# Kernel tuning notes

Measured on AMD Instinct MI355X. Metric: run time of the kernel, lower is better.

## Reference

```python
import jax, jax.numpy as jnp
import numpy as np

H, NH, NKV, HD = 4096, 32, 8, 128
GROUPS = NH // NKV            # 4
QKV_OUT = (NH + 2 * NKV) * HD # 6144
LORA_R = 256
SCALING = 1.0                 # lora_alpha / lora_r = 256/256
BLOCK_SIZE = 64


def rotate_half(x):
    d = x.shape[-1] // 2
    return jnp.concatenate([-x[..., d:], x[..., :d]], axis=-1)


def apply_rope(x, cos, sin):
    # x: [T, heads, HD]; cos/sin: [T, HD]
    return x * cos[:, None, :] + rotate_half(x) * sin[:, None, :]


def plora(x2d, w, A, B, MA, MB, im_idx, mem_idx):
    # x2d: [T, in]; w: [out, in]; A:[r,in] B:[out,r]; MA:[256,in] MB:[out,256]
    res = x2d @ w.T
    lora_im = (x2d[im_idx] @ A.T) @ B.T
    res = res.at[im_idx].add(SCALING * lora_im)
    lora_mem = (x2d[mem_idx] @ MA.T) @ MB.T
    res = res.at[mem_idx].add(SCALING * lora_mem)
    return res


def setup_inputs() -> dict:
    key = jax.random.key(0)
    ks = jax.random.split(key, 20)
    T = 2048
    inp = {
        'hidden_states': jax.random.normal(ks[0], (1, T, H), jnp.float32),
        'cos': jax.random.uniform(ks[1], (T, HD), jnp.float32, -1.0, 1.0),
        'sin': jax.random.uniform(ks[2], (T, HD), jnp.float32, -1.0, 1.0),
        'beacon_cos': jax.random.uniform(ks[3], (128, HD), jnp.float32, -1.0, 1.0),
        'beacon_sin': jax.random.uniform(ks[4], (128, HD), jnp.float32, -1.0, 1.0),
        'mem_idx': jax.random.randint(ks[5], (128,), 0, T, jnp.int32),
        'im_idx': jax.random.randint(ks[6], (512,), 0, T, jnp.int32),
        'k_cache': jnp.zeros((4, BLOCK_SIZE, NKV, HD), jnp.float32),
        'v_cache': jnp.zeros((4, BLOCK_SIZE, NKV, HD), jnp.float32),
        'block_offsets': jnp.arange(2, dtype=jnp.int32).reshape(1, 2),
        'wqkv_w': jax.random.normal(ks[7], (QKV_OUT, H), jnp.float32) * 0.02,
        'wqkv_A': jax.random.normal(ks[8], (LORA_R, H), jnp.float32) * 0.02,
        'wqkv_B': jax.random.normal(ks[9], (QKV_OUT, LORA_R), jnp.float32) * 0.02,
        'wqkv_MA': jax.random.normal(ks[10], (256, H), jnp.float32) * 0.02,
        'wqkv_MB': jax.random.normal(ks[11], (QKV_OUT, 256), jnp.float32) * 0.02,
        'wo_w': jax.random.normal(ks[12], (H, NH * HD), jnp.float32) * 0.02,
        'wo_A': jax.random.normal(ks[13], (LORA_R, NH * HD), jnp.float32) * 0.02,
        'wo_B': jax.random.normal(ks[14], (H, LORA_R), jnp.float32) * 0.02,
        'wo_MA': jax.random.normal(ks[15], (256, NH * HD), jnp.float32) * 0.02,
        'wo_MB': jax.random.normal(ks[16], (H, 256), jnp.float32) * 0.02,
    }
    return inp


def reference(hidden_states, cos, sin, beacon_cos, beacon_sin, mem_idx, im_idx,
              k_cache, v_cache, block_offsets,
              wqkv_w, wqkv_A, wqkv_B, wqkv_MA, wqkv_MB,
              wo_w, wo_A, wo_B, wo_MA, wo_MB):
    Bsz, N, C = hidden_states.shape
    x = hidden_states.reshape(-1, C)  # [T, H]
    T = x.shape[0]

    # ---- wqkv PLoRA ----
    qkv = plora(x, wqkv_w, wqkv_A, wqkv_B, wqkv_MA, wqkv_MB, im_idx, mem_idx)
    qkv = qkv.reshape(T, NKV, 2 + GROUPS, HD)
    q = qkv[:, :, :GROUPS, :].reshape(T, NH, HD)   # [T, 32, 128]
    k = qkv[:, :, -2, :]                           # [T, 8, 128]
    v = qkv[:, :, -1, :]                           # [T, 8, 128]

    # ---- fill_kv_cache: beacon tokens with beacon RoPE -> paged cache ----
    fill_k = apply_rope(k[mem_idx], beacon_cos, beacon_sin)  # [M, 8, 128]
    fill_v = v[mem_idx]
    M = fill_k.shape[0]
    pos = jnp.arange(M)
    blk = block_offsets[0, pos // BLOCK_SIZE]
    off = pos % BLOCK_SIZE
    k_cache_new = k_cache.at[blk, off].set(fill_k)
    v_cache_new = v_cache.at[blk, off].set(fill_v)

    # ---- RoPE on q/k ----
    q = apply_rope(q, cos, sin)
    k = apply_rope(k, cos, sin)

    # ---- causal GQA flash attention (single varlen sequence of length T) ----
    qg = q.reshape(T, NKV, GROUPS, HD)
    scale = 1.0 / np.sqrt(HD)
    scores = jnp.einsum('qhgd,shd->hgqs', qg, k) * scale  # [8,4,T,T]
    causal = jnp.tril(jnp.ones((T, T), dtype=bool))
    scores = jnp.where(causal[None, None], scores, jnp.finfo(scores.dtype).min)
    probs = jax.nn.softmax(scores, axis=-1)
    attn = jnp.einsum('hgqs,shd->qhgd', probs, v).reshape(T, NH * HD)

    # ---- wo PLoRA ----
    out = plora(attn, wo_w, wo_A, wo_B, wo_MA, wo_MB, im_idx, mem_idx)
    out = out.reshape(Bsz, N, H)
    return out, k_cache_new, v_cache_new
```

## Files before the change

kernel.cpp:

```cpp
#include <hip/hip_runtime.h>
#include <hip/hip_bf16.h>
#include <stdint.h>

typedef __bf16 bf16;
typedef __bf16 bf16x8 __attribute__((ext_vector_type(8)));
typedef float f32x4 __attribute__((ext_vector_type(4)));

#define T_SEQ 2048
#define NH 32
#define NKV 8
#define HD 128
#define HDIM 4096
#define QKV_OUT 6144

__device__ __forceinline__ void g2l16(const void* g, void* l) {
  __builtin_amdgcn_global_load_lds(
      (const __attribute__((address_space(1))) void*)g,
      (__attribute__((address_space(3))) void*)l, 16, 0, 0);
}

__global__ __launch_bounds__(256) void cvt_kernel(const float* __restrict__ in,
                                                  bf16* __restrict__ out, int n) {
  int stride = gridDim.x * blockDim.x * 8;
  for (int i = (blockIdx.x * blockDim.x + threadIdx.x) * 8; i < n; i += stride) {
    float4 a = *(const float4*)(in + i);
    float4 b = *(const float4*)(in + i + 4);
    bf16x8 o;
    o[0] = (bf16)a.x; o[1] = (bf16)a.y; o[2] = (bf16)a.z; o[3] = (bf16)a.w;
    o[4] = (bf16)b.x; o[5] = (bf16)b.y; o[6] = (bf16)b.z; o[7] = (bf16)b.w;
    *(bf16x8*)(out + i) = o;
  }
}

__global__ __launch_bounds__(256) void zero_f32(float* __restrict__ p, int n) {
  int i = blockIdx.x * 256 + threadIdx.x;
  if (i < n) p[i] = 0.f;
}

__global__ __launch_bounds__(256)
void gemm128(const bf16* __restrict__ A, const bf16* __restrict__ B,
             float* __restrict__ C, int M, int N, int K) {
  __shared__ bf16 As[128 * 32];
  __shared__ bf16 Bs[128 * 32];
  const int tid = threadIdx.x;
  const int wid = tid >> 6, lane = tid & 63;
  const int bm = blockIdx.x * 128, bn = blockIdx.y * 128;
  const int wr = (wid >> 1) * 64, wc = (wid & 1) * 64;
  const int lr = lane & 15, lk = (lane >> 4) * 8;
  const int srow = wid * 32 + (lane >> 2);
  const int scol = (lane & 3) * 8;
  const bf16* Ag = A + (size_t)(bm + srow) * K + scol;
  const bf16* Bg = B + (size_t)(bn + srow) * K + scol;
  bf16* Al = As + wid * 1024;
  bf16* Bl = Bs + wid * 1024;
  f32x4 acc[4][4] = {};
  for (int k0 = 0; k0 < K; k0 += 32) {
    g2l16(Ag + k0, Al);
    g2l16(Ag + k0 + (size_t)16 * K, Al + 512);
    g2l16(Bg + k0, Bl);
    g2l16(Bg + k0 + (size_t)16 * K, Bl + 512);
    __syncthreads();
    bf16x8 af[4], bfv[4];
#pragma unroll
    for (int m = 0; m < 4; ++m)
      af[m] = *(const bf16x8*)(As + (wr + m * 16 + lr) * 32 + lk);
#pragma unroll
    for (int n = 0; n < 4; ++n)
      bfv[n] = *(const bf16x8*)(Bs + (wc + n * 16 + lr) * 32 + lk);
#pragma unroll
    for (int m = 0; m < 4; ++m)
#pragma unroll
      for (int n = 0; n < 4; ++n)
        acc[m][n] = __builtin_amdgcn_mfma_f32_16x16x32_bf16(af[m], bfv[n], acc[m][n], 0, 0, 0);
    __syncthreads();
  }
  const int orow = (lane >> 4) * 4;
#pragma unroll
  for (int m = 0; m < 4; ++m)
#pragma unroll
    for (int n = 0; n < 4; ++n)
#pragma unroll
      for (int j = 0; j < 4; ++j)
        C[(size_t)(bm + wr + m * 16 + orow + j) * N + (bn + wc + n * 16 + lr)] = acc[m][n][j];
}

template <int GATHER_A, int MODE>
__global__ __launch_bounds__(256)
void gemm64(const bf16* __restrict__ A, const bf16* __restrict__ B,
            const int* __restrict__ aidx, const int* __restrict__ cidx,
            bf16* __restrict__ outb, float* __restrict__ outf,
            int M, int N, int K, int ldc, float alpha) {
  __shared__ bf16 As[64 * 32];
  __shared__ bf16 Bs[64 * 32];
  const int tid = threadIdx.x;
  const int wid = tid >> 6, lane = tid & 63;
  const int bm = blockIdx.x * 64, bn = blockIdx.y * 64;
  const int wr = (wid >> 1) * 32, wc = (wid & 1) * 32;
  const int lr = lane & 15, lk = (lane >> 4) * 8;
  int arow = bm + wid * 16 + (lane >> 2);
  if (GATHER_A) arow = aidx[arow];
  const int scol = (lane & 3) * 8;
  const bf16* Ag = A + (size_t)arow * K + scol;
  const bf16* Bg = B + (size_t)(bn + wid * 16 + (lane >> 2)) * K + scol;
  bf16* Al = As + wid * 512;
  bf16* Bl = Bs + wid * 512;
  int kbeg = 0, kend = K;
  if (MODE == 2) { int kc = K / gridDim.z; kbeg = blockIdx.z * kc; kend = kbeg + kc; }
  f32x4 acc[2][2] = {};
  for (int k0 = kbeg; k0 < kend; k0 += 32) {
    g2l16(Ag + k0, Al);
    g2l16(Bg + k0, Bl);
    __syncthreads();
    bf16x8 af[2], bfv[2];
#pragma unroll
    for (int m = 0; m < 2; ++m)
      af[m] = *(const bf16x8*)(As + (wr + m * 16 + lr) * 32 + lk);
#pragma unroll
    for (int n = 0; n < 2; ++n)
      bfv[n] = *(const bf16x8*)(Bs + (wc + n * 16 + lr) * 32 + lk);
#pragma unroll
    for (int m = 0; m < 2; ++m)
#pragma unroll
      for (int n = 0; n < 2; ++n)
        acc[m][n] = __builtin_amdgcn_mfma_f32_16x16x32_bf16(af[m], bfv[n], acc[m][n], 0, 0, 0);
    __syncthreads();
  }
  const int orow = (lane >> 4) * 4;
#pragma unroll
  for (int m = 0; m < 2; ++m)
#pragma unroll
    for (int n = 0; n < 2; ++n)
#pragma unroll
      for (int j = 0; j < 4; ++j) {
        int r = bm + wr + m * 16 + orow + j;
        int c = bn + wc + n * 16 + lr;
        float v = acc[m][n][j];
        if (MODE == 0)      outb[(size_t)r * ldc + c] = (bf16)(v * alpha);
        else if (MODE == 1) atomicAdd(outf + (size_t)cidx[r] * ldc + c, v * alpha);
        else                atomicAdd(outf + (size_t)r * ldc + c, v);
      }
}

__global__ __launch_bounds__(256)
void rope_q(const float* __restrict__ qkv, const float* __restrict__ cosp,
            const float* __restrict__ sinp, bf16* __restrict__ qb) {
  int idx = blockIdx.x * 4 + (threadIdx.x >> 6);
  int d = threadIdx.x & 63;
  int t = idx >> 5, h = idx & 31;
  const float* src = qkv + (size_t)t * QKV_OUT + (h >> 2) * 768 + (h & 3) * 128;
  float x0 = src[d], x1 = src[d + 64];
  float c0 = cosp[t * HD + d], c1 = cosp[t * HD + d + 64];
  float s0 = sinp[t * HD + d], s1 = sinp[t * HD + d + 64];
  const float SC = 0.08838834764831845f * 1.4426950408889634f;
  bf16* dst = qb + ((size_t)t * NH + h) * HD;
  dst[d]      = (bf16)((x0 * c0 - x1 * s0) * SC);
  dst[d + 64] = (bf16)((x1 * c1 + x0 * s1) * SC);
}

__global__ __launch_bounds__(256)
void rope_k(const float* __restrict__ qkv, const float* __restrict__ cosp,
            const float* __restrict__ sinp, bf16* __restrict__ kb) {
  int idx = blockIdx.x * 4 + (threadIdx.x >> 6);
  int d = threadIdx.x & 63;
  int t = idx >> 3, kvh = idx & 7;
  const float* src = qkv + (size_t)t * QKV_OUT + kvh * 768 + 512;
  float x0 = src[d], x1 = src[d + 64];
  float c0 = cosp[t * HD + d], c1 = cosp[t * HD + d + 64];
  float s0 = sinp[t * HD + d], s1 = sinp[t * HD + d + 64];
  bf16* dst = kb + ((size_t)t * NKV + kvh) * HD;
  dst[d]      = (bf16)(x0 * c0 - x1 * s0);
  dst[d + 64] = (bf16)(x1 * c1 + x0 * s1);
}

__global__ __launch_bounds__(256)
void v_trans(const float* __restrict__ qkv, bf16* __restrict__ vtb) {
  __shared__ bf16 tile[128][72];
  const int kvh = blockIdx.y;
  const int t0 = blockIdx.x * 64;
  const int tid = threadIdx.x;
  for (int i = tid; i < 64 * 32; i += 256) {
    int t = i >> 5;
    int dq = (i & 31) * 4;
    const float* p = qkv + (size_t)(t0 + t) * QKV_OUT + kvh * 768 + 640 + dq;
    float4 v = *(const float4*)p;
    tile[dq + 0][t] = (bf16)v.x;
    tile[dq + 1][t] = (bf16)v.y;
    tile[dq + 2][t] = (bf16)v.z;
    tile[dq + 3][t] = (bf16)v.w;
  }
  __syncthreads();
  for (int i = tid; i < 128 * 8; i += 256) {
    int d = i >> 3;
    int tt = (i & 7) * 8;
    bf16x8 v;
#pragma unroll
    for (int j = 0; j < 8; ++j) v[j] = tile[d][tt + j];
    *(bf16x8*)(vtb + ((size_t)kvh * HD + d) * T_SEQ + t0 + tt) = v;
  }
}

__global__ __launch_bounds__(256)
void cache_copy(const float* __restrict__ kc, const float* __restrict__ vc,
                float* __restrict__ kout, float* __restrict__ vout) {
  int i = blockIdx.x * 256 + threadIdx.x;
  kout[i] = kc[i];
  vout[i] = vc[i];
}

__global__ __launch_bounds__(256)
void cache_fill(const float* __restrict__ qkv, const int* __restrict__ mem_idx,
                const int* __restrict__ blk_off, const float* __restrict__ bcos,
                const float* __restrict__ bsin,
                float* __restrict__ kout, float* __restrict__ vout) {
  const int m = blockIdx.x;
  const int row = mem_idx[m];
  const int blk = blk_off[m >> 6];
  const int off = m & 63;
  const int tid = threadIdx.x;
  for (int i = tid; i < NKV * 64; i += 256) {
    int kvh = i >> 6, d = i & 63;
    const float* ks = qkv + (size_t)row * QKV_OUT + kvh * 768 + 512;
    const float* vs = ks + 128;
    float x0 = ks[d], x1 = ks[d + 64];
    float c0 = bcos[m * HD + d], c1 = bcos[m * HD + d + 64];
    float s0 = bsin[m * HD + d], s1 = bsin[m * HD + d + 64];
    size_t base = (((size_t)blk * 64 + off) * NKV + kvh) * HD;
    kout[base + d]      = x0 * c0 - x1 * s0;
    kout[base + d + 64] = x1 * c1 + x0 * s1;
    vout[base + d]      = vs[d];
    vout[base + d + 64] = vs[d + 64];
  }
}

__global__ __launch_bounds__(256)
void flash(const bf16* __restrict__ qb, const bf16* __restrict__ kb,
           const bf16* __restrict__ vtb, bf16* __restrict__ attnb) {
  __shared__ bf16 Ks[32 * 128];
  __shared__ bf16 Vs[128 * 32];
  __shared__ bf16 Ps[4][16 * 32];
  const int q0 = blockIdx.x * 64;
  const int h = blockIdx.y;
  const int kvh = h >> 2;
  const int tid = threadIdx.x;
  const int wid = tid >> 6, lane = tid & 63;
  const int lr = lane & 15, lg = lane >> 4;
  const int lk = lg * 8;
  bf16x8 qf[4];
  {
    const bf16* qsrc = qb + (((size_t)(q0 + wid * 16 + lr)) * NH + h) * HD + lk;
#pragma unroll
    for (int kk = 0; kk < 4; ++kk) qf[kk] = *(const bf16x8*)(qsrc + kk * 32);
  }
  f32x4 o[8] = {};
  float mrow[4] = {-1e30f, -1e30f, -1e30f, -1e30f};
  float lrow[4] = {0.f, 0.f, 0.f, 0.f};
  const int kv_end = q0 + 64;
  const int krr = wid * 8 + lg;
  const int kcb = lr * 16;
  const int vdr = wid * 32 + (lane >> 2);
  const int vcb = (lane & 3) * 16;
  for (int jt = 0; jt < kv_end; jt += 32) {
    {
      int d0 = (kcb ^ ((krr & 7) << 4)) >> 1;
      g2l16(kb + ((size_t)(jt + krr) * NKV + kvh) * HD + d0, Ks + wid * 1024);
      int rr1 = krr + 4;
      int d1 = (kcb ^ ((rr1 & 7) << 4)) >> 1;
      g2l16(kb + ((size_t)(jt + rr1) * NKV + kvh) * HD + d1, Ks + wid * 1024 + 512);
      int t0 = (vcb ^ (((vdr >> 1) & 3) << 4)) >> 1;
      g2l16(vtb + ((size_t)kvh * HD + vdr) * T_SEQ + jt + t0, Vs + wid * 1024);
      int vdr1 = vdr + 16;
      int t1 = (vcb ^ (((vdr1 >> 1) & 3) << 4)) >> 1;
      g2l16(vtb + ((size_t)kvh * HD + vdr1) * T_SEQ + jt + t1, Vs + wid * 1024 + 512);
    }
    __syncthreads();
    f32x4 S[2] = {};
    const char* KsB = (const char*)Ks;
#pragma unroll
    for (int ch = 0; ch < 2; ++ch) {
      int row = ch * 16 + lr;
      int rbase = row * 256;
      int swz = (row & 7) << 4;
#pragma unroll
      for (int kk = 0; kk < 4; ++kk) {
        bf16x8 kf = *(const bf16x8*)(KsB + rbase + ((kk * 64 + lg * 16) ^ swz));
        S[ch] = __builtin_amdgcn_mfma_f32_16x16x32_bf16(qf[kk], kf, S[ch], 0, 0, 0);
      }
    }
    const int baserow = q0 + wid * 16 + lg * 4;
    float corr[4];
#pragma unroll
    for (int j = 0; j < 4; ++j) {
      int row = baserow + j;
      float s0 = (jt + lr <= row)      ? S[0][j] : -1e30f;
      float s1 = (jt + 16 + lr <= row) ? S[1][j] : -1e30f;
      float tmx = fmaxf(s0, s1);
#pragma unroll
      for (int off = 1; off < 16; off <<= 1)
        tmx = fmaxf(tmx, __shfl_xor(tmx, off, 64));
      float mn = fmaxf(mrow[j], tmx);
      corr[j] = exp2f(mrow[j] - mn);
      mrow[j] = mn;
      float p0 = (s0 <= -1e29f) ? 0.f : exp2f(s0 - mn);
      float p1 = (s1 <= -1e29f) ? 0.f : exp2f(s1 - mn);
      S[0][j] = p0; S[1][j] = p1;
      float ps = p0 + p1;
#pragma unroll
      for (int off = 1; off < 16; off <<= 1)
        ps += __shfl_xor(ps, off, 64);
      lrow[j] = lrow[j] * corr[j] + ps;
    }
#pragma unroll
    for (int db = 0; db < 8; ++db) {
      o[db][0] *= corr[0]; o[db][1] *= corr[1];
      o[db][2] *= corr[2]; o[db][3] *= corr[3];
    }
    bf16* pw = Ps[wid];
#pragma unroll
    for (int j = 0; j < 4; ++j) {
      pw[(lg * 4 + j) * 32 + lr]      = (bf16)S[0][j];
      pw[(lg * 4 + j) * 32 + 16 + lr] = (bf16)S[1][j];
    }
    asm volatile("s_waitcnt lgkmcnt(0)" ::: "memory");
    bf16x8 pa = *(const bf16x8*)(pw + lr * 32 + lk);
    const char* VsB = (const char*)Vs;
    int vswz = ((lr >> 1) & 3) << 4;
#pragma unroll
    for (int db = 0; db < 8; ++db) {
      bf16x8 vf = *(const bf16x8*)(VsB + (db * 16 + lr) * 64 + ((lg * 16) ^ vswz));
      o[db] = __builtin_amdgcn_mfma_f32_16x16x32_bf16(pa, vf, o[db], 0, 0, 0);
    }
    __syncthreads();
  }
#pragma unroll
  for (int j = 0; j < 4; ++j) {
    float inv = 1.f / lrow[j];
    bf16* od = attnb + (((size_t)(q0 + wid * 16 + lg * 4 + j)) * NH + h) * HD;
#pragma unroll
    for (int db = 0; db < 8; ++db)
      od[db * 16 + lr] = (bf16)(o[db][j] * inv);
  }
}

extern "C" void kernel_launch(void* const* d_in, const int* in_sizes, int n_in,
                              void* d_out, int out_size, void* d_ws, size_t ws_size,
                              hipStream_t stream) {
  (void)in_sizes; (void)n_in; (void)out_size; (void)ws_size;
  const float* hidden  = (const float*)d_in[0];
  const float* cosp    = (const float*)d_in[1];
  const float* sinp    = (const float*)d_in[2];
  const float* bcos    = (const float*)d_in[3];
  const float* bsin    = (const float*)d_in[4];
  const int*   mem_idx = (const int*)d_in[5];
  const int*   im_idx  = (const int*)d_in[6];
  const float* kc_in   = (const float*)d_in[7];
  const float* vc_in   = (const float*)d_in[8];
  const int*   blk_off = (const int*)d_in[9];
  const float* wqkv_w  = (const float*)d_in[10];
  const float* wqkv_A  = (const float*)d_in[11];
  const float* wqkv_B  = (const float*)d_in[12];
  const float* wqkv_MA = (const float*)d_in[13];
  const float* wqkv_MB = (const float*)d_in[14];
  const float* wo_w    = (const float*)d_in[15];
  const float* wo_A    = (const float*)d_in[16];
  const float* wo_B    = (const float*)d_in[17];
  const float* wo_MA   = (const float*)d_in[18];
  const float* wo_MB   = (const float*)d_in[19];

  char* ws = (char*)d_ws;
  size_t off = 0;
  auto alloc = [&](size_t b) { char* p = ws + off; off += (b + 255) & ~(size_t)255; return p; };
  bf16* xb    = (bf16*)alloc(2048ull * 4096 * 2);
  bf16* wqkvb = (bf16*)alloc(6144ull * 4096 * 2);
  bf16* wob   = (bf16*)alloc(4096ull * 4096 * 2);
  bf16* qAb   = (bf16*)alloc(256ull * 4096 * 2);
  bf16* qBb   = (bf16*)alloc(6144ull * 256 * 2);
  bf16* qMAb  = (bf16*)alloc(256ull * 4096 * 2);
  bf16* qMBb  = (bf16*)alloc(6144ull * 256 * 2);
  bf16* oAb   = (bf16*)alloc(256ull * 4096 * 2);
  bf16* oBb   = (bf16*)alloc(4096ull * 256 * 2);
  bf16* oMAb  = (bf16*)alloc(256ull * 4096 * 2);
  bf16* oMBb  = (bf16*)alloc(4096ull * 256 * 2);
  float* qkv  = (float*)alloc(2048ull * 6144 * 4);
  bf16* qb    = (bf16*)alloc(2048ull * 32 * 128 * 2);
  bf16* kbuf  = (bf16*)alloc(2048ull * 8 * 128 * 2);
  bf16* vtb   = (bf16*)alloc(8ull * 128 * 2048 * 2);
  bf16* attnb = (bf16*)alloc(2048ull * 4096 * 2);
  float* tf   = (float*)alloc(1280ull * 256 * 4);
  bf16* tb    = (bf16*)alloc(1280ull * 256 * 2);
  float* t_im_f  = tf;               float* t_mem_f  = tf + 512 * 256;
  float* t2_im_f = tf + 640 * 256;   float* t2_mem_f = tf + 1152 * 256;
  bf16* t_im_b   = tb;               bf16* t_mem_b   = tb + 512 * 256;
  bf16* t2_im_b  = tb + 640 * 256;   bf16* t2_mem_b  = tb + 1152 * 256;
  (void)t_mem_f; (void)t2_mem_f;

  float* outp   = (float*)d_out;
  float* kc_out = outp + 2048ull * 4096;
  float* vc_out = kc_out + 4ull * 64 * 8 * 128;

  auto cvt = [&](const float* src, bf16* dst, size_t n) {
    size_t g = (n / 8 + 255) / 256;
    if (g > 2048) g = 2048;
    cvt_kernel<<<(unsigned)g, 256, 0, stream>>>(src, dst, (int)n);
  };
  cvt(hidden, xb, 2048ull * 4096);
  cvt(wqkv_w, wqkvb, 6144ull * 4096);
  cvt(wo_w, wob, 4096ull * 4096);
  cvt(wqkv_A, qAb, 256ull * 4096);
  cvt(wqkv_B, qBb, 6144ull * 256);
  cvt(wqkv_MA, qMAb, 256ull * 4096);
  cvt(wqkv_MB, qMBb, 6144ull * 256);
  cvt(wo_A, oAb, 256ull * 4096);
  cvt(wo_B, oBb, 4096ull * 256);
  cvt(wo_MA, oMAb, 256ull * 4096);
  cvt(wo_MB, oMBb, 4096ull * 256);
  zero_f32<<<1280, 256, 0, stream>>>(tf, 1280 * 256);

  gemm128<<<dim3(16, 48), 256, 0, stream>>>(xb, wqkvb, qkv, 2048, 6144, 4096);
  gemm64<1, 2><<<dim3(8, 4, 8), 256, 0, stream>>>(xb, qAb, im_idx, nullptr, nullptr, t_im_f, 512, 256, 4096, 256, 1.f);
  gemm64<1, 2><<<dim3(2, 4, 8), 256, 0, stream>>>(xb, qMAb, mem_idx, nullptr, nullptr, t_mem_f, 128, 256, 4096, 256, 1.f);
  cvt(tf, tb, 640 * 256);
  gemm64<0, 1><<<dim3(8, 96), 256, 0, stream>>>(t_im_b, qBb, nullptr, im_idx, nullptr, qkv, 512, 6144, 256, 6144, 1.f);
  gemm64<0, 1><<<dim3(2, 96), 256, 0, stream>>>(t_mem_b, qMBb, nullptr, mem_idx, nullptr, qkv, 128, 6144, 256, 6144, 1.f);

  rope_q<<<16384, 256, 0, stream>>>(qkv, cosp, sinp, qb);
  rope_k<<<4096, 256, 0, stream>>>(qkv, cosp, sinp, kbuf);
  v_trans<<<dim3(32, 8), 256, 0, stream>>>(qkv, vtb);
  cache_copy<<<1024, 256, 0, stream>>>(kc_in, vc_in, kc_out, vc_out);
  cache_fill<<<128, 256, 0, stream>>>(qkv, mem_idx, blk_off, bcos, bsin, kc_out, vc_out);

  flash<<<dim3(32, 32), 256, 0, stream>>>(qb, kbuf, vtb, attnb);

  gemm128<<<dim3(16, 32), 256, 0, stream>>>(attnb, wob, outp, 2048, 4096, 4096);
  gemm64<1, 2><<<dim3(8, 4, 8), 256, 0, stream>>>(attnb, oAb, im_idx, nullptr, nullptr, t2_im_f, 512, 256, 4096, 256, 1.f);
  gemm64<1, 2><<<dim3(2, 4, 8), 256, 0, stream>>>(attnb, oMAb, mem_idx, nullptr, nullptr, t2_mem_f, 128, 256, 4096, 256, 1.f);
  cvt(t2_im_f, t2_im_b, 640 * 256);
  gemm64<0, 1><<<dim3(8, 64), 256, 0, stream>>>(t2_im_b, oBb, nullptr, im_idx, nullptr, outp, 512, 4096, 256, 4096, 1.f);
  gemm64<0, 1><<<dim3(2, 64), 256, 0, stream>>>(t2_mem_b, oMBb, nullptr, mem_idx, nullptr, outp, 128, 4096, 256, 4096, 1.f);
}
```

Before: 913.2 us.

## Restructure flash attention with 128-row Q tiles, 64-key blocks and register P

The flash attention kernel now gives each block 128 query rows (32 per wave, as two 16-row sub-tiles) and loads 64 keys per iteration, so each K/V tile in shared memory is reused by twice as many rows. It computes S transposed (K times Q), so every lane owns one query row and softmax reductions need only two cross-lane shuffles. The probability tile is repacked into the MFMA operand layout with register shuffles rather than a round trip through shared memory. Blocks run the heaviest causal tiles first, waves skip fully masked key blocks, and masking is applied only on diagonal tiles. The trade-offs are higher register pressure and half as many blocks in the grid.

```diff
diff --git a/kernel.cpp b/kernel.cpp
--- a/kernel.cpp
+++ b/kernel.cpp
@@ -4,6 +4,7 @@
 
 typedef __bf16 bf16;
 typedef __bf16 bf16x8 __attribute__((ext_vector_type(8)));
+typedef __bf16 bf16x4 __attribute__((ext_vector_type(4)));
 typedef float f32x4 __attribute__((ext_vector_type(4)));
 
 #define T_SEQ 2048
@@ -232,112 +233,166 @@
   }
 }
 
+__device__ __forceinline__ uint32_t pk2(float x, float y) {
+  bf16 a = (bf16)x, b = (bf16)y;
+  uint16_t ua = __builtin_bit_cast(uint16_t, a), ub = __builtin_bit_cast(uint16_t, b);
+  return (uint32_t)ua | ((uint32_t)ub << 16);
+}
+
+__device__ __forceinline__ bf16x8 dance(const f32x4& pc0, const f32x4& pc1, int lg) {
+  uint32_t a0 = pk2(pc0[0], pc0[1]), a1 = pk2(pc0[2], pc0[3]);
+  uint32_t b0 = pk2(pc1[0], pc1[1]), b1 = pk2(pc1[2], pc1[3]);
+  bool lo = lg < 2;
+  uint32_t k0 = lo ? a0 : b0, k1 = lo ? a1 : b1;
+  uint32_t s0 = lo ? b0 : a0, s1 = lo ? b1 : a1;
+  uint32_t r0 = (uint32_t)__shfl_xor((int)s0, 32, 64);
+  uint32_t r1 = (uint32_t)__shfl_xor((int)s1, 32, 64);
+  uint32_t tk0 = (uint32_t)__shfl_xor((int)k0, 16, 64);
+  uint32_t tk1 = (uint32_t)__shfl_xor((int)k1, 16, 64);
+  uint32_t tr0 = (uint32_t)__shfl_xor((int)r0, 16, 64);
+  uint32_t tr1 = (uint32_t)__shfl_xor((int)r1, 16, 64);
+  bool ev = !(lg & 1);
+  union { uint32_t u[4]; bf16x8 v; } out;
+  out.u[0] = ev ? (lo ? k0 : r0) : (lo ? tr0 : tk0);
+  out.u[1] = ev ? (lo ? k1 : r1) : (lo ? tr1 : tk1);
+  out.u[2] = ev ? (lo ? tk0 : tr0) : (lo ? r0 : k0);
+  out.u[3] = ev ? (lo ? tk1 : tr1) : (lo ? r1 : k1);
+  return out.v;
+}
+
+__device__ __forceinline__ float online_sm(f32x4 (&S)[4], float& m_r, float& l_r) {
+  float pmax = S[0][0];
+#pragma unroll
+  for (int ch = 0; ch < 4; ++ch)
+#pragma unroll
+    for (int j = 0; j < 4; ++j) pmax = fmaxf(pmax, S[ch][j]);
+  pmax = fmaxf(pmax, __shfl_xor(pmax, 16, 64));
+  pmax = fmaxf(pmax, __shfl_xor(pmax, 32, 64));
+  float mn = fmaxf(m_r, pmax);
+  float corr = exp2f(m_r - mn);
+  m_r = mn;
+  float ps = 0.f;
+#pragma unroll
+  for (int ch = 0; ch < 4; ++ch)
+#pragma unroll
+    for (int j = 0; j < 4; ++j) {
+      float p = exp2f(S[ch][j] - mn);
+      S[ch][j] = p;
+      ps += p;
+    }
+  ps += __shfl_xor(ps, 16, 64);
+  ps += __shfl_xor(ps, 32, 64);
+  l_r = l_r * corr + ps;
+  return corr;
+}
+
 __global__ __launch_bounds__(256)
 void flash(const bf16* __restrict__ qb, const bf16* __restrict__ kb,
            const bf16* __restrict__ vtb, bf16* __restrict__ attnb) {
-  __shared__ bf16 Ks[32 * 128];
-  __shared__ bf16 Vs[128 * 32];
-  __shared__ bf16 Ps[4][16 * 32];
-  const int q0 = blockIdx.x * 64;
+  __shared__ bf16 Ks[64 * 128];
+  __shared__ bf16 Vs[128 * 64];
+  const int qt = gridDim.x - 1 - blockIdx.x;
+  const int q0 = qt * 128;
   const int h = blockIdx.y;
   const int kvh = h >> 2;
   const int tid = threadIdx.x;
   const int wid = tid >> 6, lane = tid & 63;
   const int lr = lane & 15, lg = lane >> 4;
-  const int lk = lg * 8;
-  bf16x8 qf[4];
+  const int qrowA = q0 + wid * 32 + lr;
+  const int qrowB = qrowA + 16;
+
+  bf16x8 qfA[4], qfB[4];
   {
-    const bf16* qsrc = qb + (((size_t)(q0 + wid * 16 + lr)) * NH + h) * HD + lk;
-#pragma unroll
-    for (int kk = 0; kk < 4; ++kk) qf[kk] = *(const bf16x8*)(qsrc + kk * 32);
-  }
-  f32x4 o[8] = {};
-  float mrow[4] = {-1e30f, -1e30f, -1e30f, -1e30f};
-  float lrow[4] = {0.f, 0.f, 0.f, 0.f};
-  const int kv_end = q0 + 64;
-  const int krr = wid * 8 + lg;
-  const int kcb = lr * 16;
-  const int vdr = wid * 32 + (lane >> 2);
-  const int vcb = (lane & 3) * 16;
-  for (int jt = 0; jt < kv_end; jt += 32) {
-    {
-      int d0 = (kcb ^ ((krr & 7) << 4)) >> 1;
-      g2l16(kb + ((size_t)(jt + krr) * NKV + kvh) * HD + d0, Ks + wid * 1024);
-      int rr1 = krr + 4;
-      int d1 = (kcb ^ ((rr1 & 7) << 4)) >> 1;
-      g2l16(kb + ((size_t)(jt + rr1) * NKV + kvh) * HD + d1, Ks + wid * 1024 + 512);
-      int t0 = (vcb ^ (((vdr >> 1) & 3) << 4)) >> 1;
-      g2l16(vtb + ((size_t)kvh * HD + vdr) * T_SEQ + jt + t0, Vs + wid * 1024);
-      int vdr1 = vdr + 16;
-      int t1 = (vcb ^ (((vdr1 >> 1) & 3) << 4)) >> 1;
-      g2l16(vtb + ((size_t)kvh * HD + vdr1) * T_SEQ + jt + t1, Vs + wid * 1024 + 512);
+    const bf16* qa = qb + (((size_t)qrowA) * NH + h) * HD + lg * 8;
+    const bf16* qc = qb + (((size_t)qrowB) * NH + h) * HD + lg * 8;
+#pragma unroll
+    for (int kk = 0; kk < 4; ++kk) {
+      qfA[kk] = *(const bf16x8*)(qa + kk * 32);
+      qfB[kk] = *(const bf16x8*)(qc + kk * 32);
     }
-    __syncthreads();
-    f32x4 S[2] = {};
-    const char* KsB = (const char*)Ks;
-#pragma unroll
-    for (int ch = 0; ch < 2; ++ch) {
-      int row = ch * 16 + lr;
-      int rbase = row * 256;
-      int swz = (row & 7) << 4;
-#pragma unroll
-      for (int kk = 0; kk < 4; ++kk) {
-        bf16x8 kf = *(const bf16x8*)(KsB + rbase + ((kk * 64 + lg * 16) ^ swz));
-        S[ch] = __builtin_amdgcn_mfma_f32_16x16x32_bf16(qf[kk], kf, S[ch], 0, 0, 0);
+  }
+  f32x4 oA[8] = {}, oB[8] = {};
+  float mA = -1e30f, lA = 0.f, mB = -1e30f, lB = 0.f;
+
+  const int k_r0 = wid * 16 + lg;
+  const int k_cb = lr * 16;
+  const int v_r0 = wid * 32 + (lane >> 3);
+  const int v_cb = (lane & 7) * 16;
+
+  const int kv_end = q0 + 128;
+  for (int jt = 0; jt < kv_end; jt += 64) {
+#pragma unroll
+    for (int i = 0; i < 4; ++i) {
+      const int krow = k_r0 + i * 4;
+      g2l16(kb + ((size_t)(jt + krow) * NKV + kvh) * HD + ((k_cb ^ ((krow & 7) << 4)) >> 1),
+            Ks + wid * 2048 + i * 512);
+      const int vrow = v_r0 + i * 8;
+      g2l16(vtb + ((size_t)kvh * HD + vrow) * T_SEQ + jt + ((v_cb ^ ((vrow & 7) << 4)) >> 1),
+            Vs + wid * 2048 + i * 512);
+    }
+    __syncthreads();
+    if (jt <= q0 + wid * 32 + 31) {
+      const char* KsB = (const char*)Ks;
+      f32x4 SA[4] = {}, SB[4] = {};
+#pragma unroll
+      for (int ch = 0; ch < 4; ++ch) {
+        const int row = ch * 16 + lr;
+        const char* rb = KsB + row * 256;
+        const int swz = (row & 7) << 4;
+#pragma unroll
+        for (int kk = 0; kk < 4; ++kk) {
+          bf16x8 kf = *(const bf16x8*)(rb + ((kk * 64 + lg * 16) ^ swz));
+          SA[ch] = __builtin_amdgcn_mfma_f32_16x16x32_bf16(kf, qfA[kk], SA[ch], 0, 0, 0);
+          SB[ch] = __builtin_amdgcn_mfma_f32_16x16x32_bf16(kf, qfB[kk], SB[ch], 0, 0, 0);
+        }
+      }
+      if (jt + 63 > q0 + wid * 32) {
+#pragma unroll
+        for (int ch = 0; ch < 4; ++ch)
+#pragma unroll
+          for (int j = 0; j < 4; ++j) {
+            const int kv = jt + ch * 16 + lg * 4 + j;
+            if (kv > qrowA) SA[ch][j] = -1e30f;
+            if (kv > qrowB) SB[ch][j] = -1e30f;
+          }
+      }
+      float corrA = online_sm(SA, mA, lA);
+      float corrB = online_sm(SB, mB, lB);
+#pragma unroll
+      for (int db = 0; db < 8; ++db) { oA[db] *= corrA; oB[db] *= corrB; }
+      bf16x8 pbA[2], pbB[2];
+#pragma unroll
+      for (int ks = 0; ks < 2; ++ks) {
+        pbA[ks] = dance(SA[2 * ks], SA[2 * ks + 1], lg);
+        pbB[ks] = dance(SB[2 * ks], SB[2 * ks + 1], lg);
+      }
+      const char* VsB = (const char*)Vs;
+#pragma unroll
+      for (int db = 0; db < 8; ++db) {
+        const int row = db * 16 + lr;
+        const char* rb = VsB + row * 128;
+        const int swz = (row & 7) << 4;
+#pragma unroll
+        for (int ks = 0; ks < 2; ++ks) {
+          bf16x8 vf = *(const bf16x8*)(rb + ((ks * 64 + lg * 16) ^ swz));
+          oA[db] = __builtin_amdgcn_mfma_f32_16x16x32_bf16(vf, pbA[ks], oA[db], 0, 0, 0);
+          oB[db] = __builtin_amdgcn_mfma_f32_16x16x32_bf16(vf, pbB[ks], oB[db], 0, 0, 0);
+        }
       }
     }
-    const int baserow = q0 + wid * 16 + lg * 4;
-    float corr[4];
+    __syncthreads();
+  }
+  const float invA = 1.f / lA, invB = 1.f / lB;
+#pragma unroll
+  for (int db = 0; db < 8; ++db) {
+    bf16x4 wA, wB;
 #pragma unroll
     for (int j = 0; j < 4; ++j) {
-      int row = baserow + j;
-      float s0 = (jt + lr <= row)      ? S[0][j] : -1e30f;
-      float s1 = (jt + 16 + lr <= row) ? S[1][j] : -1e30f;
-      float tmx = fmaxf(s0, s1);
-#pragma unroll
-      for (int off = 1; off < 16; off <<= 1)
-        tmx = fmaxf(tmx, __shfl_xor(tmx, off, 64));
-      float mn = fmaxf(mrow[j], tmx);
-      corr[j] = exp2f(mrow[j] - mn);
-      mrow[j] = mn;
-      float p0 = (s0 <= -1e29f) ? 0.f : exp2f(s0 - mn);
-      float p1 = (s1 <= -1e29f) ? 0.f : exp2f(s1 - mn);
-      S[0][j] = p0; S[1][j] = p1;
-      float ps = p0 + p1;
-#pragma unroll
-      for (int off = 1; off < 16; off <<= 1)
-        ps += __shfl_xor(ps, off, 64);
-      lrow[j] = lrow[j] * corr[j] + ps;
+      wA[j] = (bf16)(oA[db][j] * invA);
+      wB[j] = (bf16)(oB[db][j] * invB);
     }
-#pragma unroll
-    for (int db = 0; db < 8; ++db) {
-      o[db][0] *= corr[0]; o[db][1] *= corr[1];
-      o[db][2] *= corr[2]; o[db][3] *= corr[3];
-    }
-    bf16* pw = Ps[wid];
-#pragma unroll
-    for (int j = 0; j < 4; ++j) {
-      pw[(lg * 4 + j) * 32 + lr]      = (bf16)S[0][j];
-      pw[(lg * 4 + j) * 32 + 16 + lr] = (bf16)S[1][j];
-    }
-    asm volatile("s_waitcnt lgkmcnt(0)" ::: "memory");
-    bf16x8 pa = *(const bf16x8*)(pw + lr * 32 + lk);
-    const char* VsB = (const char*)Vs;
-    int vswz = ((lr >> 1) & 3) << 4;
-#pragma unroll
-    for (int db = 0; db < 8; ++db) {
-      bf16x8 vf = *(const bf16x8*)(VsB + (db * 16 + lr) * 64 + ((lg * 16) ^ vswz));
-      o[db] = __builtin_amdgcn_mfma_f32_16x16x32_bf16(pa, vf, o[db], 0, 0, 0);
-    }
-    __syncthreads();
-  }
-#pragma unroll
-  for (int j = 0; j < 4; ++j) {
-    float inv = 1.f / lrow[j];
-    bf16* od = attnb + (((size_t)(q0 + wid * 16 + lg * 4 + j)) * NH + h) * HD;
-#pragma unroll
-    for (int db = 0; db < 8; ++db)
-      od[db * 16 + lr] = (bf16)(o[db][j] * inv);
+    *(bf16x4*)(attnb + (size_t)qrowA * HDIM + h * HD + db * 16 + lg * 4) = wA;
+    *(bf16x4*)(attnb + (size_t)qrowB * HDIM + h * HD + db * 16 + lg * 4) = wB;
   }
 }
 
@@ -428,7 +483,7 @@
   cache_copy<<<1024, 256, 0, stream>>>(kc_in, vc_in, kc_out, vc_out);
   cache_fill<<<128, 256, 0, stream>>>(qkv, mem_idx, blk_off, bcos, bsin, kc_out, vc_out);
 
-  flash<<<dim3(32, 32), 256, 0, stream>>>(qb, kbuf, vtb, attnb);
+  flash<<<dim3(16, 32), 256, 0, stream>>>(qb, kbuf, vtb, attnb);
 
   gemm128<<<dim3(16, 32), 256, 0, stream>>>(attnb, wob, outp, 2048, 4096, 4096);
   gemm64<1, 2><<<dim3(8, 4, 8), 256, 0, stream>>>(attnb, oAb, im_idx, nullptr, nullptr, t2_im_f, 512, 256, 4096, 256, 1.f);
```

Result: faster. 882.3 us (-3.4%).
